# Optimization experiments

Measured on AMD Instinct MI355X. Metric: run time of the kernel, lower is better.

Reference implementation:

```python
import jax, jax.numpy as jnp
import numpy as np

N, D_IN, D_ATTN = 8192, 48, 8


def setup_inputs() -> dict:
    key = jax.random.key(0)
    ks = jax.random.split(key, 9)
    s = 1.0 / np.sqrt(D_IN)
    return {
        "x": jax.random.normal(ks[0], (N, D_IN), jnp.float32),
        "Kw": jax.random.normal(ks[1], (D_IN, D_ATTN), jnp.float32) * s,
        "Kb": jax.random.normal(ks[2], (D_ATTN,), jnp.float32) * s,
        "Qw": jax.random.normal(ks[3], (D_IN, D_ATTN), jnp.float32) * s,
        "Qb": jax.random.normal(ks[4], (D_ATTN,), jnp.float32) * s,
        "Vw": jax.random.normal(ks[5], (D_IN, D_ATTN), jnp.float32) * s,
        "Vb": jax.random.normal(ks[6], (D_ATTN,), jnp.float32) * s,
        "Zw": jax.random.normal(ks[7], (D_ATTN, D_IN), jnp.float32) * (1.0 / np.sqrt(D_ATTN)),
        "Zb": jax.random.normal(ks[8], (D_IN,), jnp.float32) * (1.0 / np.sqrt(D_ATTN)),
    }


def reference(x, Kw, Kb, Qw, Qb, Vw, Vb, Zw, Zb):
    # Tiny QKV projections: [N,48] -> [N,8]
    Xk = x @ Kw + Kb
    Xq = x @ Qw + Qb
    Xv = x @ Vw + Vb
    # Attention over the batch/row dimension: [N,8]@[8,N] -> [N,N]
    scale = jnp.sqrt(jnp.asarray(D_ATTN, jnp.float32))
    AM = jax.nn.softmax(Xk @ Xq.T / scale, axis=1)  # torch F.softmax 2D default dim=1
    Z = AM @ Xv                                      # [N,8]
    return x + (Z @ Zw + Zb)                         # residual + output proj [N,48]
```

## Files before the change

### kernel.cpp

```cpp
#include <hip/hip_runtime.h>
#include <hip/hip_fp16.h>


#define QV_OFF   32768
#define BMAX_OFF 98304
#define PART_OFF 98560

union HU2 { unsigned u; __half2 h; };

static __device__ __forceinline__ unsigned pku(float a, float b) {
    auto v = __builtin_amdgcn_cvt_pkrtz(a, b);
    union { decltype(v) v2; unsigned u; } t;
    t.v2 = v;
    return t.u;
}
static __device__ __forceinline__ __half2 asH2(unsigned u) {
    HU2 t; t.u = u; return t.h;
}

__global__ __launch_bounds__(256) void proj_kernel(
    const float* __restrict__ x,
    const float* __restrict__ Kw, const float* __restrict__ Kb,
    const float* __restrict__ Qw, const float* __restrict__ Qb,
    const float* __restrict__ Vw, const float* __restrict__ Vb,
    unsigned* __restrict__ Xksf16, unsigned* __restrict__ QV,
    float* __restrict__ bmax)
{
    __shared__ float xs[32 * 49];
    __shared__ float wAll[3 * 388];
    __shared__ float bs[24];
    __shared__ float outv[32][25];
    const int tid = threadIdx.x;
    const int r0 = blockIdx.x * 32;

    for (int i = tid; i < 1536; i += 256) {
        int r = i / 48, c = i - r * 48;
        xs[r * 49 + c] = x[r0 * 48 + i];
    }
    for (int i = tid; i < 384; i += 256) {
        wAll[i]       = Kw[i];
        wAll[388 + i] = Qw[i];
        wAll[776 + i] = Vw[i];
    }
    if (tid < 8)       bs[tid] = Kb[tid];
    else if (tid < 16) bs[tid] = Qb[tid - 8];
    else if (tid < 24) bs[tid] = Vb[tid - 16];
    __syncthreads();

    const int rl = tid >> 3;
    const int g  = tid & 7;
    const int c0 = 3 * g;
    const float* xr = &xs[rl * 49];
    const float* w0 = &wAll[((c0 + 0) >> 3) * 388 + ((c0 + 0) & 7)];
    const float* w1 = &wAll[((c0 + 1) >> 3) * 388 + ((c0 + 1) & 7)];
    const float* w2 = &wAll[((c0 + 2) >> 3) * 388 + ((c0 + 2) & 7)];
    float a0 = bs[c0], a1 = bs[c0 + 1], a2 = bs[c0 + 2];
    #pragma unroll
    for (int k = 0; k < 48; k++) {
        const float xv = xr[k];
        a0 = fmaf(xv, w0[k * 8], a0);
        a1 = fmaf(xv, w1[k * 8], a1);
        a2 = fmaf(xv, w2[k * 8], a2);
    }
    outv[rl][c0] = a0; outv[rl][c0 + 1] = a1; outv[rl][c0 + 2] = a2;
    __syncthreads();

    {
        const int p = tid >> 4;
        const int c = (tid >> 1) & 7;
        const int m = tid & 1;
        const int col = (m ? 16 : 8) + c;
        QV[(blockIdx.x * 16 + p) * 16 + m * 8 + c] =
            pku(outv[2 * p][col], outv[2 * p + 1][col]);
    }
    const float kscale = 0.51008732149f;
    if (tid < 32) {
        uint4 o;
        o.x = pku(outv[tid][0] * kscale, outv[tid][1] * kscale);
        o.y = pku(outv[tid][2] * kscale, outv[tid][3] * kscale);
        o.z = pku(outv[tid][4] * kscale, outv[tid][5] * kscale);
        o.w = pku(outv[tid][6] * kscale, outv[tid][7] * kscale);
        ((uint4*)Xksf16)[r0 + tid] = o;
    }
    if (tid >= 192 && tid < 224) {
        const int r = tid - 192;
        float n2 = 0.f;
        #pragma unroll
        for (int c = 0; c < 8; c++) n2 = fmaf(outv[r][8 + c], outv[r][8 + c], n2);
        #pragma unroll
        for (int off = 16; off > 0; off >>= 1)
            n2 = fmaxf(n2, __shfl_xor(n2, off, 64));
        if (r == 0) bmax[blockIdx.x] = n2;
    }
}

__global__ __launch_bounds__(256) void attn_kernel(
    const unsigned* __restrict__ Xksf16, const unsigned* __restrict__ QV,
    const float* __restrict__ bmax,
    __half* __restrict__ partH, int P)
{
    __shared__ uint4 tile[256];
    const int tid  = threadIdx.x;
    const int lane = tid & 63;
    const int wv   = tid >> 6;
    const int g    = blockIdx.x & 7;
    const int ch   = blockIdx.x >> 3;

    float m = fmaxf(fmaxf(bmax[lane], bmax[64 + lane]),
                    fmaxf(bmax[128 + lane], bmax[192 + lane]));
    #pragma unroll
    for (int off = 32; off > 0; off >>= 1)
        m = fmaxf(m, __shfl_xor(m, off, 64));
    const float qmax2 = m;

    const int rbase = g * 1024 + wv * 256 + lane;
    __half2 k2b[4][8];
    __half2 sinit2[4], l2[4], acc2[4][8];
    const __half2 zero2 = __float2half2_rn(0.f);
    const __half2 one2  = __float2half2_rn(1.f);
    #pragma unroll
    for (int k = 0; k < 4; k++) {
        const uint4 kv = ((const uint4*)Xksf16)[rbase + 64 * k];
        const __half2 k01 = asH2(kv.x), k23 = asH2(kv.y),
                      k45 = asH2(kv.z), k67 = asH2(kv.w);
        k2b[k][0] = __low2half2(k01);  k2b[k][1] = __high2half2(k01);
        k2b[k][2] = __low2half2(k23);  k2b[k][3] = __high2half2(k23);
        k2b[k][4] = __low2half2(k45);  k2b[k][5] = __high2half2(k45);
        k2b[k][6] = __low2half2(k67);  k2b[k][7] = __high2half2(k67);
        float kn2 = 0.f;
        #pragma unroll
        for (int c = 0; c < 8; c++) {
            const float kf = __low2float(k2b[k][c]);
            kn2 = fmaf(kf, kf, kn2);
        }
        sinit2[k] = __float2half2_rn(-sqrtf(kn2 * qmax2));
        l2[k] = zero2;
        #pragma unroll
        for (int c = 0; c < 8; c++) acc2[k][c] = zero2;
    }

    for (int t0 = 0; t0 < P; t0 += 64) {
        const int np = (P - t0 < 64) ? (P - t0) : 64;
        __syncthreads();
        for (int i = tid; i < np * 4; i += 256)
            tile[i] = ((const uint4*)QV)[((size_t)ch * P + t0) * 4 + i];
        __syncthreads();

        #pragma unroll 4
        for (int p = 0; p < np; p++) {
            const uint4 qp0 = tile[p * 4 + 0];
            const uint4 qp1 = tile[p * 4 + 1];
            const uint4 vp0 = tile[p * 4 + 2];
            const uint4 vp1 = tile[p * 4 + 3];
            const __half2 q0 = asH2(qp0.x), q1 = asH2(qp0.y),
                          q2 = asH2(qp0.z), q3 = asH2(qp0.w),
                          q4 = asH2(qp1.x), q5 = asH2(qp1.y),
                          q6 = asH2(qp1.z), q7 = asH2(qp1.w);
            const __half2 v0 = asH2(vp0.x), v1 = asH2(vp0.y),
                          v2 = asH2(vp0.z), v3 = asH2(vp0.w),
                          v4 = asH2(vp1.x), v5 = asH2(vp1.y),
                          v6 = asH2(vp1.z), v7 = asH2(vp1.w);
            #pragma unroll
            for (int k = 0; k < 4; k++) {
                __half2 s2 = sinit2[k];
                s2 = __hfma2(k2b[k][0], q0, s2);
                s2 = __hfma2(k2b[k][1], q1, s2);
                s2 = __hfma2(k2b[k][2], q2, s2);
                s2 = __hfma2(k2b[k][3], q3, s2);
                s2 = __hfma2(k2b[k][4], q4, s2);
                s2 = __hfma2(k2b[k][5], q5, s2);
                s2 = __hfma2(k2b[k][6], q6, s2);
                s2 = __hfma2(k2b[k][7], q7, s2);
                const float p0 = __builtin_amdgcn_exp2f(__low2float(s2));
                const float p1 = __builtin_amdgcn_exp2f(__high2float(s2));
                const __half2 ph = asH2(pku(p0, p1));
                l2[k] = __hfma2(ph, one2, l2[k]);
                acc2[k][0] = __hfma2(ph, v0, acc2[k][0]);
                acc2[k][1] = __hfma2(ph, v1, acc2[k][1]);
                acc2[k][2] = __hfma2(ph, v2, acc2[k][2]);
                acc2[k][3] = __hfma2(ph, v3, acc2[k][3]);
                acc2[k][4] = __hfma2(ph, v4, acc2[k][4]);
                acc2[k][5] = __hfma2(ph, v5, acc2[k][5]);
                acc2[k][6] = __hfma2(ph, v6, acc2[k][6]);
                acc2[k][7] = __hfma2(ph, v7, acc2[k][7]);
            }
        }
    }

    #pragma unroll
    for (int k = 0; k < 4; k++) {
        const int row = rbase + 64 * k;
        #pragma unroll
        for (int c = 0; c < 8; c++) {
            const float af = __low2float(acc2[k][c]) + __high2float(acc2[k][c]);
            partH[((size_t)(ch * 9 + c) << 13) + row] = __float2half_rn(af);
        }
        const float lf = __low2float(l2[k]) + __high2float(l2[k]);
        partH[((size_t)(ch * 9 + 8) << 13) + row] = __float2half_rn(lf);
    }
}

__global__ __launch_bounds__(256) void finish_kernel(
    const float* __restrict__ x,
    const float* __restrict__ Zw, const float* __restrict__ Zb,
    const __half* __restrict__ partH, float* __restrict__ out, int nch)
{
    __shared__ float red[4][64][10];
    __shared__ float Zs[64][9];
    __shared__ float zw_s[384];
    __shared__ float zb_s[48];
    const int tid = threadIdx.x;
    const int r0 = blockIdx.x * 64;

    for (int i = tid; i < 384; i += 256) zw_s[i] = Zw[i];
    if (tid < 48) zb_s[tid] = Zb[tid];

    const int r = tid & 63, s = tid >> 6;
    const int row = r0 + r;
    const int cps = nch >> 2;
    float a[9];
    #pragma unroll
    for (int c = 0; c < 9; c++) a[c] = 0.f;
    for (int i = 0; i < cps; i++) {
        const int ch = s * cps + i;
        const __half* p = partH + ((size_t)(ch * 9) << 13) + row;
        #pragma unroll
        for (int c = 0; c < 9; c++) a[c] += __half2float(p[(size_t)c << 13]);
    }
    #pragma unroll
    for (int c = 0; c < 9; c++) red[s][r][c] = a[c];
    __syncthreads();
    if (tid < 64) {
        float b[9];
        #pragma unroll
        for (int c = 0; c < 9; c++)
            b[c] = red[0][tid][c] + red[1][tid][c] + red[2][tid][c] + red[3][tid][c];
        const float inv = 1.0f / b[8];
        #pragma unroll
        for (int c = 0; c < 8; c++) Zs[tid][c] = b[c] * inv;
    }
    __syncthreads();

    for (int e = tid; e < 64 * 48; e += 256) {
        const int rr = e / 48, c = e - rr * 48;
        float o = x[r0 * 48 + e] + zb_s[c];
        #pragma unroll
        for (int k = 0; k < 8; k++) o = fmaf(Zs[rr][k], zw_s[k * 48 + c], o);
        out[r0 * 48 + e] = o;
    }
}

extern "C" void kernel_launch(void* const* d_in, const int* in_sizes, int n_in,
                              void* d_out, int out_size, void* d_ws, size_t ws_size,
                              hipStream_t stream) {
    const float* x  = (const float*)d_in[0];
    const float* Kw = (const float*)d_in[1];
    const float* Kb = (const float*)d_in[2];
    const float* Qw = (const float*)d_in[3];
    const float* Qb = (const float*)d_in[4];
    const float* Vw = (const float*)d_in[5];
    const float* Vb = (const float*)d_in[6];
    const float* Zw = (const float*)d_in[7];
    const float* Zb = (const float*)d_in[8];
    float* out = (float*)d_out;

    float* ws = (float*)d_ws;
    unsigned* Xksf16 = (unsigned*)ws;
    unsigned* QV     = (unsigned*)(ws + QV_OFF);
    float* bmax      = ws + BMAX_OFF;
    __half* partH    = (__half*)(ws + PART_OFF);

    int nch = 128;
    while (nch > 4 &&
           (size_t)PART_OFF * 4 + (size_t)nch * 9 * 8192 * 2 > ws_size) nch >>= 1;
    const int P = 4096 / nch;

    proj_kernel<<<256, 256, 0, stream>>>(x, Kw, Kb, Qw, Qb, Vw, Vb,
                                         Xksf16, QV, bmax);
    attn_kernel<<<8 * nch, 256, 0, stream>>>(Xksf16, QV, bmax, partH, P);
    finish_kernel<<<128, 256, 0, stream>>>(x, Zw, Zb, partH, out, nch);
}
```

Measured before the change: 127.5 us.

## Shrink attention blocks to single wave and use inline packed fp16 FMA

Restructures attn_kernel from 256-thread blocks (4 waves sharing a 64-key tile) into 64-thread single-wave blocks, with four times as many blocks and 32-key tiles loaded by the lone wave. The QKV inner loop now calls v_pk_fma_f16 through inline asm on raw packed registers, and the key broadcasts are prebuilt with integer duplication. The aim is to cut barrier cost and give the scheduler finer-grained work while avoiding __half2 wrapper overhead. In exchange, each loaded Q/V tile is reused by fewer waves, so LDS loads per FMA go up. The tile loop also assumes P is a multiple of 32.

```diff
diff --git a/kernel.cpp b/kernel.cpp
--- a/kernel.cpp
+++ b/kernel.cpp
@@ -6,16 +6,22 @@
 #define BMAX_OFF 98304
 #define PART_OFF 98560
 
-union HU2 { unsigned u; __half2 h; };
+typedef _Float16 hv2 __attribute__((ext_vector_type(2)));
+union HVU { unsigned u; hv2 v; };
 
 static __device__ __forceinline__ unsigned pku(float a, float b) {
-    auto v = __builtin_amdgcn_cvt_pkrtz(a, b);
-    union { decltype(v) v2; unsigned u; } t;
-    t.v2 = v;
-    return t.u;
-}
-static __device__ __forceinline__ __half2 asH2(unsigned u) {
-    HU2 t; t.u = u; return t.h;
+    auto t = __builtin_amdgcn_cvt_pkrtz(a, b);
+    union { decltype(t) x; unsigned u; } c; c.x = t; return c.u;
+}
+static __device__ __forceinline__ hv2 asV(unsigned u) { HVU t; t.u = u; return t.v; }
+static __device__ __forceinline__ unsigned dupL(unsigned u) {
+    const unsigned lo = u & 0xFFFFu; return lo | (lo << 16);
+}
+static __device__ __forceinline__ unsigned dupH(unsigned u) {
+    const unsigned hi = u >> 16; return hi | (hi << 16);
+}
+static __device__ __forceinline__ void pkfma(unsigned& d, unsigned a, unsigned b) {
+    asm("v_pk_fma_f16 %0, %1, %2, %0" : "+v"(d) : "v"(a), "v"(b));
 }
 
 __global__ __launch_bounds__(256) void proj_kernel(
@@ -94,17 +100,15 @@
     }
 }
 
-__global__ __launch_bounds__(256) void attn_kernel(
+__global__ __launch_bounds__(64) void attn_kernel(
     const unsigned* __restrict__ Xksf16, const unsigned* __restrict__ QV,
     const float* __restrict__ bmax,
     __half* __restrict__ partH, int P)
 {
-    __shared__ uint4 tile[256];
-    const int tid  = threadIdx.x;
-    const int lane = tid & 63;
-    const int wv   = tid >> 6;
-    const int g    = blockIdx.x & 7;
-    const int ch   = blockIdx.x >> 3;
+    __shared__ uint4 tile4[128];
+    const int lane  = threadIdx.x;
+    const int g     = blockIdx.x & 31;
+    const int chunk = blockIdx.x >> 5;
 
     float m = fmaxf(fmaxf(bmax[lane], bmax[64 + lane]),
                     fmaxf(bmax[128 + lane], bmax[192 + lane]));
@@ -113,90 +117,81 @@
         m = fmaxf(m, __shfl_xor(m, off, 64));
     const float qmax2 = m;
 
-    const int rbase = g * 1024 + wv * 256 + lane;
-    __half2 k2b[4][8];
-    __half2 sinit2[4], l2[4], acc2[4][8];
-    const __half2 zero2 = __float2half2_rn(0.f);
-    const __half2 one2  = __float2half2_rn(1.f);
+    unsigned kd[4][8], sinit2[4], l2[4], acc[4][8];
     #pragma unroll
     for (int k = 0; k < 4; k++) {
-        const uint4 kv = ((const uint4*)Xksf16)[rbase + 64 * k];
-        const __half2 k01 = asH2(kv.x), k23 = asH2(kv.y),
-                      k45 = asH2(kv.z), k67 = asH2(kv.w);
-        k2b[k][0] = __low2half2(k01);  k2b[k][1] = __high2half2(k01);
-        k2b[k][2] = __low2half2(k23);  k2b[k][3] = __high2half2(k23);
-        k2b[k][4] = __low2half2(k45);  k2b[k][5] = __high2half2(k45);
-        k2b[k][6] = __low2half2(k67);  k2b[k][7] = __high2half2(k67);
+        const int row = g * 256 + k * 64 + lane;
+        const uint4 kv = ((const uint4*)Xksf16)[row];
+        kd[k][0] = dupL(kv.x); kd[k][1] = dupH(kv.x);
+        kd[k][2] = dupL(kv.y); kd[k][3] = dupH(kv.y);
+        kd[k][4] = dupL(kv.z); kd[k][5] = dupH(kv.z);
+        kd[k][6] = dupL(kv.w); kd[k][7] = dupH(kv.w);
         float kn2 = 0.f;
         #pragma unroll
         for (int c = 0; c < 8; c++) {
-            const float kf = __low2float(k2b[k][c]);
+            const float kf = (float)asV(kd[k][c]).x;
             kn2 = fmaf(kf, kf, kn2);
         }
-        sinit2[k] = __float2half2_rn(-sqrtf(kn2 * qmax2));
-        l2[k] = zero2;
-        #pragma unroll
-        for (int c = 0; c < 8; c++) acc2[k][c] = zero2;
-    }
-
-    for (int t0 = 0; t0 < P; t0 += 64) {
-        const int np = (P - t0 < 64) ? (P - t0) : 64;
+        const float sinit = -sqrtf(kn2 * qmax2);
+        sinit2[k] = pku(sinit, sinit);
+        l2[k] = 0u;
+        #pragma unroll
+        for (int c = 0; c < 8; c++) acc[k][c] = 0u;
+    }
+    const unsigned one2 = 0x3C003C00u;
+
+    for (int t0 = 0; t0 < P; t0 += 32) {
         __syncthreads();
-        for (int i = tid; i < np * 4; i += 256)
-            tile[i] = ((const uint4*)QV)[((size_t)ch * P + t0) * 4 + i];
+        tile4[lane]      = ((const uint4*)QV)[((size_t)chunk * P + t0) * 4 + lane];
+        tile4[lane + 64] = ((const uint4*)QV)[((size_t)chunk * P + t0) * 4 + lane + 64];
         __syncthreads();
 
-        #pragma unroll 4
-        for (int p = 0; p < np; p++) {
-            const uint4 qp0 = tile[p * 4 + 0];
-            const uint4 qp1 = tile[p * 4 + 1];
-            const uint4 vp0 = tile[p * 4 + 2];
-            const uint4 vp1 = tile[p * 4 + 3];
-            const __half2 q0 = asH2(qp0.x), q1 = asH2(qp0.y),
-                          q2 = asH2(qp0.z), q3 = asH2(qp0.w),
-                          q4 = asH2(qp1.x), q5 = asH2(qp1.y),
-                          q6 = asH2(qp1.z), q7 = asH2(qp1.w);
-            const __half2 v0 = asH2(vp0.x), v1 = asH2(vp0.y),
-                          v2 = asH2(vp0.z), v3 = asH2(vp0.w),
-                          v4 = asH2(vp1.x), v5 = asH2(vp1.y),
-                          v6 = asH2(vp1.z), v7 = asH2(vp1.w);
+        #pragma unroll 2
+        for (int p = 0; p < 32; p++) {
+            const uint4 qp0 = tile4[p * 4 + 0];
+            const uint4 qp1 = tile4[p * 4 + 1];
+            const uint4 vp0 = tile4[p * 4 + 2];
+            const uint4 vp1 = tile4[p * 4 + 3];
             #pragma unroll
             for (int k = 0; k < 4; k++) {
-                __half2 s2 = sinit2[k];
-                s2 = __hfma2(k2b[k][0], q0, s2);
-                s2 = __hfma2(k2b[k][1], q1, s2);
-                s2 = __hfma2(k2b[k][2], q2, s2);
-                s2 = __hfma2(k2b[k][3], q3, s2);
-                s2 = __hfma2(k2b[k][4], q4, s2);
-                s2 = __hfma2(k2b[k][5], q5, s2);
-                s2 = __hfma2(k2b[k][6], q6, s2);
-                s2 = __hfma2(k2b[k][7], q7, s2);
-                const float p0 = __builtin_amdgcn_exp2f(__low2float(s2));
-                const float p1 = __builtin_amdgcn_exp2f(__high2float(s2));
-                const __half2 ph = asH2(pku(p0, p1));
-                l2[k] = __hfma2(ph, one2, l2[k]);
-                acc2[k][0] = __hfma2(ph, v0, acc2[k][0]);
-                acc2[k][1] = __hfma2(ph, v1, acc2[k][1]);
-                acc2[k][2] = __hfma2(ph, v2, acc2[k][2]);
-                acc2[k][3] = __hfma2(ph, v3, acc2[k][3]);
-                acc2[k][4] = __hfma2(ph, v4, acc2[k][4]);
-                acc2[k][5] = __hfma2(ph, v5, acc2[k][5]);
-                acc2[k][6] = __hfma2(ph, v6, acc2[k][6]);
-                acc2[k][7] = __hfma2(ph, v7, acc2[k][7]);
+                unsigned s2 = sinit2[k];
+                pkfma(s2, kd[k][0], qp0.x);
+                pkfma(s2, kd[k][1], qp0.y);
+                pkfma(s2, kd[k][2], qp0.z);
+                pkfma(s2, kd[k][3], qp0.w);
+                pkfma(s2, kd[k][4], qp1.x);
+                pkfma(s2, kd[k][5], qp1.y);
+                pkfma(s2, kd[k][6], qp1.z);
+                pkfma(s2, kd[k][7], qp1.w);
+                const hv2 sv = asV(s2);
+                const float pa = __builtin_amdgcn_exp2f((float)sv.x);
+                const float pb = __builtin_amdgcn_exp2f((float)sv.y);
+                const unsigned ph = pku(pa, pb);
+                pkfma(l2[k], ph, one2);
+                pkfma(acc[k][0], ph, vp0.x);
+                pkfma(acc[k][1], ph, vp0.y);
+                pkfma(acc[k][2], ph, vp0.z);
+                pkfma(acc[k][3], ph, vp0.w);
+                pkfma(acc[k][4], ph, vp1.x);
+                pkfma(acc[k][5], ph, vp1.y);
+                pkfma(acc[k][6], ph, vp1.z);
+                pkfma(acc[k][7], ph, vp1.w);
             }
         }
     }
 
     #pragma unroll
     for (int k = 0; k < 4; k++) {
-        const int row = rbase + 64 * k;
+        const int row = g * 256 + k * 64 + lane;
         #pragma unroll
         for (int c = 0; c < 8; c++) {
-            const float af = __low2float(acc2[k][c]) + __high2float(acc2[k][c]);
-            partH[((size_t)(ch * 9 + c) << 13) + row] = __float2half_rn(af);
+            const hv2 a = asV(acc[k][c]);
+            partH[((size_t)(chunk * 9 + c) << 13) + row] =
+                __float2half_rn((float)a.x + (float)a.y);
         }
-        const float lf = __low2float(l2[k]) + __high2float(l2[k]);
-        partH[((size_t)(ch * 9 + 8) << 13) + row] = __float2half_rn(lf);
+        const hv2 lv = asV(l2[k]);
+        partH[((size_t)(chunk * 9 + 8) << 13) + row] =
+            __float2half_rn((float)lv.x + (float)lv.y);
     }
 }
 
@@ -277,6 +272,6 @@
 
     proj_kernel<<<256, 256, 0, stream>>>(x, Kw, Kb, Qw, Qb, Vw, Vb,
                                          Xksf16, QV, bmax);
-    attn_kernel<<<8 * nch, 256, 0, stream>>>(Xksf16, QV, bmax, partH, P);
+    attn_kernel<<<32 * nch, 64, 0, stream>>>(Xksf16, QV, bmax, partH, P);
     finish_kernel<<<128, 256, 0, stream>>>(x, Zw, Zb, partH, out, nch);
 }
```

Result: no change. 128.1 us (+0.5%).
